# Performance work log

Hardware: AMD Instinct MI355X
Metric: run time of the kernel (lower is better)

The kernel has to match this reference:

```python
import jax, jax.numpy as jnp
import numpy as np

N = 100000      # nodes
E = 1600000     # edges (unique, no self-loops)
DIN = 128
DOUT = 128


def _make_edges():
    """Unique undirected edges, no self-loops, ring guarantees min degree 2.
    Ensures dense-adjacency semantics == edge-list segment-sum semantics."""
    rng = np.random.default_rng(0)
    ring = np.stack([np.arange(N, dtype=np.int64), (np.arange(N, dtype=np.int64) + 1) % N], axis=1)
    ring = np.sort(ring, axis=1)  # canonical (min,max)
    ring_keys = ring[:, 0] * N + ring[:, 1]
    cand = rng.integers(0, N, size=(3 * E, 2), dtype=np.int64)
    cand = cand[cand[:, 0] != cand[:, 1]]
    cand = np.sort(cand, axis=1)
    keys = cand[:, 0] * N + cand[:, 1]
    _, idx = np.unique(keys, return_index=True)
    cand = cand[np.sort(idx)]
    cand = cand[~np.isin(cand[:, 0] * N + cand[:, 1], ring_keys)][: E - N]
    edges = np.concatenate([ring, cand], axis=0)  # [E, 2]
    return edges.T  # [2, E]


def setup_inputs() -> dict:
    key = jax.random.key(0)
    kx, kw = jax.random.split(key)
    X = jax.random.normal(kx, (N, DIN), dtype=jnp.float32)
    # kaiming_normal_ default (fan_in mode): std = sqrt(2 / fan_in)
    W = jax.random.normal(kw, (DIN, DOUT), dtype=jnp.float32) * np.float32(np.sqrt(2.0 / DIN))
    edge_list = jnp.asarray(_make_edges(), dtype=jnp.int64)
    return {"X": X, "W": W, "edge_list": edge_list}


def reference(X, W, edge_list):
    src, dst = edge_list[0], edge_list[1]
    n = X.shape[0]
    ones = jnp.ones(src.shape[0], dtype=X.dtype)
    # D: each edge increments both endpoint degrees (matches the torch loop)
    deg = jnp.zeros((n,), X.dtype).at[src].add(ones).at[dst].add(ones)
    # A_hat @ X = symmetric neighbor aggregation + self (identity)
    agg = jnp.zeros_like(X).at[dst].add(X[src]).at[src].add(X[dst]) + X
    # D^-1 is inverse of diagonal -> elementwise reciprocal
    z = (agg / deg[:, None]) @ W
    return jax.nn.relu(z)
```

## Files before the change

### kernel.cpp

```cpp
#include <hip/hip_runtime.h>
#include <hip/hip_fp16.h>


#define DFEAT 128
#define BSH 7
#define BNODES (1 << BSH)
#define NBMAX 800
#define EPB 8192
#define SORT_CAP 6144

typedef __attribute__((ext_vector_type(8))) short short8;
typedef __attribute__((ext_vector_type(4))) float f32x4;

__device__ __forceinline__ unsigned short f2bf(float x) {
  unsigned u = __float_as_uint(x);
  return (unsigned short)((u + 0x7FFFu + ((u >> 16) & 1u)) >> 16);
}
__device__ __forceinline__ __half2 u2h(unsigned x) {
  union { unsigned u; __half2 h; } c; c.u = x; return c.h;
}

__global__ void init_kernel(const int* el32, int* gcur, int* flag, int NB) {
  int i = blockIdx.x * blockDim.x + threadIdx.x;
  if (i < NB) gcur[i] = 0;
  if (i == 0) flag[0] = (el32[1] == 0 && el32[3] == 0) ? 1 : 0;
}

__device__ __forceinline__ int edge_at(const void* el, long long i, int mode64) {
  if (mode64) return (int)((const long long*)el)[i];
  return ((const int*)el)[i];
}

__global__ __launch_bounds__(1024) void scatter_kernel(const void* el,
                                                       const int* __restrict__ flag,
                                                       int* __restrict__ gcur,
                                                       unsigned int* __restrict__ bucket,
                                                       int E, int NB) {
  __shared__ int lh[NBMAX];
  __shared__ int lb[NBMAX];
  int t = threadIdx.x;
  for (int i = t; i < NB; i += 1024) lh[i] = 0;
  __syncthreads();
  int m = flag[0];
  long long e0 = (long long)blockIdx.x * EPB + t;
  int s[8], d[8];
#pragma unroll
  for (int r = 0; r < 8; r++) {
    long long e = e0 + r * 1024;
    if (e < E) {
      s[r] = edge_at(el, e, m);
      d[r] = edge_at(el, (long long)E + e, m);
    } else {
      s[r] = -1;
    }
  }
#pragma unroll
  for (int r = 0; r < 8; r++) {
    if (s[r] >= 0) {
      atomicAdd(&lh[s[r] >> BSH], 1);
      atomicAdd(&lh[d[r] >> BSH], 1);
    }
  }
  __syncthreads();
  for (int i = t; i < NB; i += 1024) {
    int c = lh[i];
    lb[i] = c ? atomicAdd(&gcur[i], c) : 0;
  }
  __syncthreads();
  for (int i = t; i < NB; i += 1024) lh[i] = 0;
  __syncthreads();
#pragma unroll
  for (int r = 0; r < 8; r++) {
    if (s[r] >= 0) {
      int bs = s[r] >> BSH, bd = d[r] >> BSH;
      int ps = lb[bs] + atomicAdd(&lh[bs], 1);
      if (ps < SORT_CAP)
        bucket[(long long)bs * SORT_CAP + ps] =
            ((unsigned)(s[r] & (BNODES - 1)) << 20) | (unsigned)d[r];
      int pd = lb[bd] + atomicAdd(&lh[bd], 1);
      if (pd < SORT_CAP)
        bucket[(long long)bd * SORT_CAP + pd] =
            ((unsigned)(d[r] & (BNODES - 1)) << 20) | (unsigned)s[r];
    }
  }
}

__global__ __launch_bounds__(256) void wfrag_kernel(const float* __restrict__ W,
                                                    unsigned int* __restrict__ Wfrag) {
  int e = blockIdx.x * 256 + threadIdx.x;
  if (e >= 2048) return;
  int lane = e & 63;
  int nt = (e >> 6) & 7;
  int kc = e >> 9;
  int k0 = kc * 32 + (lane >> 4) * 8;
  int col = nt * 16 + (lane & 15);
  unsigned int o[4];
#pragma unroll
  for (int jj = 0; jj < 4; jj++) {
    unsigned short lo = f2bf(W[(k0 + 2 * jj) * DFEAT + col]);
    unsigned short hi = f2bf(W[(k0 + 2 * jj + 1) * DFEAT + col]);
    o[jj] = (unsigned)lo | ((unsigned)hi << 16);
  }
  uint4* dst = (uint4*)Wfrag;
  uint4 v; v.x = o[0]; v.y = o[1]; v.z = o[2]; v.w = o[3];
  dst[e] = v;
}

__global__ __launch_bounds__(256) void gemm_kernel(const float* __restrict__ X,
                                                   const short8* __restrict__ Wfrag,
                                                   __half* __restrict__ Yh, int n) {
  int wave = threadIdx.x >> 6;
  int lane = threadIdx.x & 63;
  int row0 = (blockIdx.x * 4 + wave) * 16;
  if (row0 >= n) return;

  int rowA = row0 + (lane & 15);
  if (rowA >= n) rowA = n - 1;
  const float4* Xrow = (const float4*)(X + (long long)rowA * DFEAT);
  int koff = (lane >> 4) * 2;

  f32x4 acc[8];
#pragma unroll
  for (int ntp = 0; ntp < 8; ntp++) acc[ntp] = (f32x4){0.f, 0.f, 0.f, 0.f};

#pragma unroll
  for (int kc = 0; kc < 4; kc++) {
    float4 xa = Xrow[kc * 8 + koff];
    float4 xb = Xrow[kc * 8 + koff + 1];
    short8 a8;
    a8[0] = (short)f2bf(xa.x); a8[1] = (short)f2bf(xa.y);
    a8[2] = (short)f2bf(xa.z); a8[3] = (short)f2bf(xa.w);
    a8[4] = (short)f2bf(xb.x); a8[5] = (short)f2bf(xb.y);
    a8[6] = (short)f2bf(xb.z); a8[7] = (short)f2bf(xb.w);
#pragma unroll
    for (int nt = 0; nt < 8; nt++) {
      short8 b8 = Wfrag[(kc * 8 + nt) * 64 + lane];
      acc[nt] = __builtin_amdgcn_mfma_f32_16x16x32_bf16(a8, b8, acc[nt], 0, 0, 0);
    }
  }

  int rbase = row0 + (lane >> 4) * 4;
  int cbase = lane & 15;
#pragma unroll
  for (int nt = 0; nt < 8; nt++) {
#pragma unroll
    for (int r = 0; r < 4; r++) {
      int row = rbase + r;
      if (row < n)
        Yh[(long long)row * DFEAT + nt * 16 + cbase] = __float2half(acc[nt][r]);
    }
  }
}

__global__ __launch_bounds__(1024, 8) void gather_kernel(const __half* __restrict__ Yh,
                                                         const int* __restrict__ gcur,
                                                         const unsigned int* __restrict__ bucket,
                                                         float* __restrict__ out, int n) {
  __shared__ unsigned int srt[SORT_CAP];
  __shared__ int h[BNODES], pref[BNODES], cur[BNODES], scn[BNODES];
  int b = blockIdx.x, t = threadIdx.x;
  int cnt = gcur[b]; if (cnt > SORT_CAP) cnt = SORT_CAP;
  long long base = (long long)b * SORT_CAP;

  if (t < BNODES) h[t] = 0;
  __syncthreads();
  for (int i = t; i < cnt; i += 1024)
    atomicAdd(&h[bucket[base + i] >> 20], 1);
  __syncthreads();
  int v = (t < BNODES) ? h[t] : 0;
  if (t < BNODES) scn[t] = v;
  __syncthreads();
  for (int dd = 1; dd < BNODES; dd <<= 1) {
    int a = (t < BNODES && t >= dd) ? scn[t - dd] : 0;
    __syncthreads();
    if (t < BNODES) scn[t] += a;
    __syncthreads();
  }
  if (t < BNODES) { pref[t] = scn[t] - v; cur[t] = scn[t] - v; }
  __syncthreads();
  for (int i = t; i < cnt; i += 1024) {
    unsigned e = bucket[base + i];
    int p = atomicAdd(&cur[e >> 20], 1);
    srt[p] = e & 0xFFFFFu;
  }
  __syncthreads();

  int wv = t >> 6, lane = t & 63;
  int sub = lane >> 4, fl = lane & 15;
  const uint4* Y4 = (const uint4*)Yh;

  for (int oo = 0; oo < 8; oo++) {
    int o = wv * 8 + oo;
    int node = (b << BSH) + o;
    if (node >= n) break;
    int start = pref[o], len = h[o];

    __half2 a0 = u2h(0), a1 = u2h(0), a2 = u2h(0), a3 = u2h(0);
    if (sub == 0) {
      uint4 u = Y4[(long long)node * 16 + fl];
      a0 = __hadd2(a0, u2h(u.x)); a1 = __hadd2(a1, u2h(u.y));
      a2 = __hadd2(a2, u2h(u.z)); a3 = __hadd2(a3, u2h(u.w));
    }
    int i = sub;
    for (; i + 4 < len; i += 8) {
      unsigned j0 = srt[start + i];
      unsigned j1 = srt[start + i + 4];
      uint4 u0 = Y4[(long long)j0 * 16 + fl];
      uint4 u1 = Y4[(long long)j1 * 16 + fl];
      a0 = __hadd2(a0, u2h(u0.x)); a1 = __hadd2(a1, u2h(u0.y));
      a2 = __hadd2(a2, u2h(u0.z)); a3 = __hadd2(a3, u2h(u0.w));
      a0 = __hadd2(a0, u2h(u1.x)); a1 = __hadd2(a1, u2h(u1.y));
      a2 = __hadd2(a2, u2h(u1.z)); a3 = __hadd2(a3, u2h(u1.w));
    }
    if (i < len) {
      unsigned j0 = srt[start + i];
      uint4 u0 = Y4[(long long)j0 * 16 + fl];
      a0 = __hadd2(a0, u2h(u0.x)); a1 = __hadd2(a1, u2h(u0.y));
      a2 = __hadd2(a2, u2h(u0.z)); a3 = __hadd2(a3, u2h(u0.w));
    }

    float2 f0 = __half22float2(a0), f1 = __half22float2(a1);
    float2 f2 = __half22float2(a2), f3 = __half22float2(a3);
    float g[8] = {f0.x, f0.y, f1.x, f1.y, f2.x, f2.y, f3.x, f3.y};
#pragma unroll
    for (int k = 0; k < 8; k++) {
      g[k] += __shfl_xor(g[k], 16);
      g[k] += __shfl_xor(g[k], 32);
    }
    if (sub == 0) {
      float inv = 1.0f / (float)len;
      float4 o0, o1;
      o0.x = g[0] * inv; o0.y = g[1] * inv; o0.z = g[2] * inv; o0.w = g[3] * inv;
      o1.x = g[4] * inv; o1.y = g[5] * inv; o1.z = g[6] * inv; o1.w = g[7] * inv;
      o0.x = o0.x > 0.f ? o0.x : 0.f; o0.y = o0.y > 0.f ? o0.y : 0.f;
      o0.z = o0.z > 0.f ? o0.z : 0.f; o0.w = o0.w > 0.f ? o0.w : 0.f;
      o1.x = o1.x > 0.f ? o1.x : 0.f; o1.y = o1.y > 0.f ? o1.y : 0.f;
      o1.z = o1.z > 0.f ? o1.z : 0.f; o1.w = o1.w > 0.f ? o1.w : 0.f;
      float4* op = (float4*)(out + (long long)node * DFEAT);
      op[fl * 2] = o0;
      op[fl * 2 + 1] = o1;
    }
  }
}

extern "C" void kernel_launch(void* const* d_in, const int* in_sizes, int n_in,
                              void* d_out, int out_size, void* d_ws, size_t ws_size,
                              hipStream_t stream) {
  const float* X = (const float*)d_in[0];
  const float* W = (const float*)d_in[1];
  const void* el = d_in[2];
  float* out = (float*)d_out;

  int n = in_sizes[0] / DFEAT;
  int E = in_sizes[2] / 2;
  int NB = (n + BNODES - 1) >> BSH;

  char* p = (char*)d_ws;
  auto alloc = [&](size_t bytes) -> char* {
    char* q = p;
    p += (bytes + 511) & ~(size_t)511;
    return q;
  };
  int* gcur = (int*)alloc((size_t)NBMAX * 4);
  int* flag = (int*)alloc(64);
  unsigned int* bucket = (unsigned int*)alloc((size_t)NBMAX * SORT_CAP * 4);
  unsigned int* Wfrag = (unsigned int*)alloc((size_t)2048 * 16);
  __half* Yh = (__half*)alloc((size_t)n * DFEAT * 2);

  int eblocks = (E + EPB - 1) / EPB;

  init_kernel<<<(NBMAX + 255) / 256, 256, 0, stream>>>((const int*)el, gcur, flag, NB);
  scatter_kernel<<<eblocks, 1024, 0, stream>>>(el, flag, gcur, bucket, E, NB);
  wfrag_kernel<<<8, 256, 0, stream>>>(W, Wfrag);
  gemm_kernel<<<(n + 63) / 64, 256, 0, stream>>>(X, (const short8*)Wfrag, Yh, n);
  gather_kernel<<<NB, 1024, 0, stream>>>(Yh, gcur, bucket, out, n);
}
```

Before: 273.0 us.

## Split bucket sort into separate CSR kernel and use wave-per-node gather

```diff
diff --git a/kernel.cpp b/kernel.cpp
--- a/kernel.cpp
+++ b/kernel.cpp
@@ -85,6 +85,48 @@
   }
 }
 
+__global__ __launch_bounds__(1024) void sort_kernel(const unsigned int* __restrict__ bucket,
+                                                    const int* __restrict__ gcur,
+                                                    int* __restrict__ adj,
+                                                    int* __restrict__ start,
+                                                    int* __restrict__ degg,
+                                                    int n) {
+  __shared__ int srt[SORT_CAP];
+  __shared__ int h[BNODES], pref[BNODES], cur[BNODES], scn[BNODES];
+  int b = blockIdx.x, t = threadIdx.x;
+  int cnt = gcur[b]; if (cnt > SORT_CAP) cnt = SORT_CAP;
+  long long base = (long long)b * SORT_CAP;
+
+  if (t < BNODES) h[t] = 0;
+  __syncthreads();
+  for (int i = t; i < cnt; i += 1024)
+    atomicAdd(&h[bucket[base + i] >> 20], 1);
+  __syncthreads();
+  int v = (t < BNODES) ? h[t] : 0;
+  if (t < BNODES) scn[t] = v;
+  __syncthreads();
+  for (int dd = 1; dd < BNODES; dd <<= 1) {
+    int a = (t < BNODES && t >= dd) ? scn[t - dd] : 0;
+    __syncthreads();
+    if (t < BNODES) scn[t] += a;
+    __syncthreads();
+  }
+  if (t < BNODES) { pref[t] = scn[t] - v; cur[t] = scn[t] - v; }
+  __syncthreads();
+  for (int i = t; i < cnt; i += 1024) {
+    unsigned e = bucket[base + i];
+    int p = atomicAdd(&cur[e >> 20], 1);
+    srt[p] = (int)(e & 0xFFFFFu);
+  }
+  __syncthreads();
+  for (int i = t; i < cnt; i += 1024) adj[base + i] = srt[i];
+  int node = (b << BSH) + t;
+  if (t < BNODES && node < n) {
+    start[node] = (int)(base + pref[t]);
+    degg[node] = h[t];
+  }
+}
+
 __global__ __launch_bounds__(256) void wfrag_kernel(const float* __restrict__ W,
                                                     unsigned int* __restrict__ Wfrag) {
   int e = blockIdx.x * 256 + threadIdx.x;
@@ -152,95 +194,50 @@
   }
 }
 
-__global__ __launch_bounds__(1024, 8) void gather_kernel(const __half* __restrict__ Yh,
-                                                         const int* __restrict__ gcur,
-                                                         const unsigned int* __restrict__ bucket,
-                                                         float* __restrict__ out, int n) {
-  __shared__ unsigned int srt[SORT_CAP];
-  __shared__ int h[BNODES], pref[BNODES], cur[BNODES], scn[BNODES];
-  int b = blockIdx.x, t = threadIdx.x;
-  int cnt = gcur[b]; if (cnt > SORT_CAP) cnt = SORT_CAP;
-  long long base = (long long)b * SORT_CAP;
-
-  if (t < BNODES) h[t] = 0;
-  __syncthreads();
-  for (int i = t; i < cnt; i += 1024)
-    atomicAdd(&h[bucket[base + i] >> 20], 1);
-  __syncthreads();
-  int v = (t < BNODES) ? h[t] : 0;
-  if (t < BNODES) scn[t] = v;
-  __syncthreads();
-  for (int dd = 1; dd < BNODES; dd <<= 1) {
-    int a = (t < BNODES && t >= dd) ? scn[t - dd] : 0;
-    __syncthreads();
-    if (t < BNODES) scn[t] += a;
-    __syncthreads();
-  }
-  if (t < BNODES) { pref[t] = scn[t] - v; cur[t] = scn[t] - v; }
-  __syncthreads();
-  for (int i = t; i < cnt; i += 1024) {
-    unsigned e = bucket[base + i];
-    int p = atomicAdd(&cur[e >> 20], 1);
-    srt[p] = e & 0xFFFFFu;
-  }
-  __syncthreads();
-
-  int wv = t >> 6, lane = t & 63;
-  int sub = lane >> 4, fl = lane & 15;
-  const uint4* Y4 = (const uint4*)Yh;
-
-  for (int oo = 0; oo < 8; oo++) {
-    int o = wv * 8 + oo;
-    int node = (b << BSH) + o;
-    if (node >= n) break;
-    int start = pref[o], len = h[o];
-
-    __half2 a0 = u2h(0), a1 = u2h(0), a2 = u2h(0), a3 = u2h(0);
-    if (sub == 0) {
-      uint4 u = Y4[(long long)node * 16 + fl];
-      a0 = __hadd2(a0, u2h(u.x)); a1 = __hadd2(a1, u2h(u.y));
-      a2 = __hadd2(a2, u2h(u.z)); a3 = __hadd2(a3, u2h(u.w));
-    }
-    int i = sub;
-    for (; i + 4 < len; i += 8) {
-      unsigned j0 = srt[start + i];
-      unsigned j1 = srt[start + i + 4];
-      uint4 u0 = Y4[(long long)j0 * 16 + fl];
-      uint4 u1 = Y4[(long long)j1 * 16 + fl];
-      a0 = __hadd2(a0, u2h(u0.x)); a1 = __hadd2(a1, u2h(u0.y));
-      a2 = __hadd2(a2, u2h(u0.z)); a3 = __hadd2(a3, u2h(u0.w));
-      a0 = __hadd2(a0, u2h(u1.x)); a1 = __hadd2(a1, u2h(u1.y));
-      a2 = __hadd2(a2, u2h(u1.z)); a3 = __hadd2(a3, u2h(u1.w));
-    }
-    if (i < len) {
-      unsigned j0 = srt[start + i];
-      uint4 u0 = Y4[(long long)j0 * 16 + fl];
-      a0 = __hadd2(a0, u2h(u0.x)); a1 = __hadd2(a1, u2h(u0.y));
-      a2 = __hadd2(a2, u2h(u0.z)); a3 = __hadd2(a3, u2h(u0.w));
-    }
-
-    float2 f0 = __half22float2(a0), f1 = __half22float2(a1);
-    float2 f2 = __half22float2(a2), f3 = __half22float2(a3);
-    float g[8] = {f0.x, f0.y, f1.x, f1.y, f2.x, f2.y, f3.x, f3.y};
-#pragma unroll
-    for (int k = 0; k < 8; k++) {
-      g[k] += __shfl_xor(g[k], 16);
-      g[k] += __shfl_xor(g[k], 32);
-    }
-    if (sub == 0) {
-      float inv = 1.0f / (float)len;
-      float4 o0, o1;
-      o0.x = g[0] * inv; o0.y = g[1] * inv; o0.z = g[2] * inv; o0.w = g[3] * inv;
-      o1.x = g[4] * inv; o1.y = g[5] * inv; o1.z = g[6] * inv; o1.w = g[7] * inv;
-      o0.x = o0.x > 0.f ? o0.x : 0.f; o0.y = o0.y > 0.f ? o0.y : 0.f;
-      o0.z = o0.z > 0.f ? o0.z : 0.f; o0.w = o0.w > 0.f ? o0.w : 0.f;
-      o1.x = o1.x > 0.f ? o1.x : 0.f; o1.y = o1.y > 0.f ? o1.y : 0.f;
-      o1.z = o1.z > 0.f ? o1.z : 0.f; o1.w = o1.w > 0.f ? o1.w : 0.f;
-      float4* op = (float4*)(out + (long long)node * DFEAT);
-      op[fl * 2] = o0;
-      op[fl * 2 + 1] = o1;
-    }
-  }
+__global__ __launch_bounds__(256) void gather_kernel(const unsigned int* __restrict__ Yh,
+                                                     const int* __restrict__ start,
+                                                     const int* __restrict__ degg,
+                                                     const int* __restrict__ adj,
+                                                     float2* __restrict__ out2, int n) {
+  int wid = (int)((blockIdx.x * (long long)blockDim.x + threadIdx.x) >> 6);
+  int lane = threadIdx.x & 63;
+  if (wid >= n) return;
+
+  int off0 = start[wid], len = degg[wid];
+  __half2 acc0 = u2h(Yh[(long long)wid * 64 + lane]);
+  __half2 acc1 = u2h(0);
+
+  for (int base = 0; base < len; base += 64) {
+    int cnt = len - base; if (cnt > 64) cnt = 64;
+    int idx = (lane < cnt) ? adj[off0 + base + lane] : 0;
+    int t = 0;
+    for (; t + 8 <= cnt; t += 8) {
+      unsigned v[8];
+#pragma unroll
+      for (int u = 0; u < 8; u++) {
+        int j = __shfl(idx, t + u);
+        v[u] = Yh[(long long)j * 64 + lane];
+      }
+      acc0 = __hadd2(acc0, u2h(v[0])); acc1 = __hadd2(acc1, u2h(v[1]));
+      acc0 = __hadd2(acc0, u2h(v[2])); acc1 = __hadd2(acc1, u2h(v[3]));
+      acc0 = __hadd2(acc0, u2h(v[4])); acc1 = __hadd2(acc1, u2h(v[5]));
+      acc0 = __hadd2(acc0, u2h(v[6])); acc1 = __hadd2(acc1, u2h(v[7]));
+    }
+    for (; t < cnt; t++) {
+      int j = __shfl(idx, t);
+      acc0 = __hadd2(acc0, u2h(Yh[(long long)j * 64 + lane]));
+    }
+  }
+
+  float2 f0 = __half22float2(acc0);
+  float2 f1 = __half22float2(acc1);
+  float inv = 1.0f / (float)len;
+  float2 o;
+  o.x = (f0.x + f1.x) * inv;
+  o.y = (f0.y + f1.y) * inv;
+  o.x = o.x > 0.f ? o.x : 0.f;
+  o.y = o.y > 0.f ? o.y : 0.f;
+  out2[(long long)wid * 64 + lane] = o;
 }
 
 extern "C" void kernel_launch(void* const* d_in, const int* in_sizes, int n_in,
@@ -264,6 +261,9 @@
   int* gcur = (int*)alloc((size_t)NBMAX * 4);
   int* flag = (int*)alloc(64);
   unsigned int* bucket = (unsigned int*)alloc((size_t)NBMAX * SORT_CAP * 4);
+  int* adj   = (int*)alloc((size_t)NBMAX * SORT_CAP * 4);
+  int* start = (int*)alloc((size_t)n * 4);
+  int* degg  = (int*)alloc((size_t)n * 4);
   unsigned int* Wfrag = (unsigned int*)alloc((size_t)2048 * 16);
   __half* Yh = (__half*)alloc((size_t)n * DFEAT * 2);
 
@@ -271,7 +271,9 @@
 
   init_kernel<<<(NBMAX + 255) / 256, 256, 0, stream>>>((const int*)el, gcur, flag, NB);
   scatter_kernel<<<eblocks, 1024, 0, stream>>>(el, flag, gcur, bucket, E, NB);
+  sort_kernel<<<NB, 1024, 0, stream>>>(bucket, gcur, adj, start, degg, n);
   wfrag_kernel<<<8, 256, 0, stream>>>(W, Wfrag);
   gemm_kernel<<<(n + 63) / 64, 256, 0, stream>>>(X, (const short8*)Wfrag, Yh, n);
-  gather_kernel<<<NB, 1024, 0, stream>>>(Yh, gcur, bucket, out, n);
-}
+  gather_kernel<<<(n + 3) / 4, 256, 0, stream>>>((const unsigned int*)Yh, start, degg,
+                                                 adj, (float2*)out, n);
+}
```

Result: faster. 267.0 us (-2.2%).
